# Kernel tuning notes

Measured on AMD Instinct MI355X. Metric: run time of the kernel, lower is better.

The kernel has to match this reference:

```python
import jax, jax.numpy as jnp
import numpy as np

B, N, D, H, F = 2, 2048, 1024, 16, 4096
E = D // H
EPS = 1e-5

def layer_norm(x, g, b):
    mu = jnp.mean(x, axis=-1, keepdims=True)
    var = jnp.var(x, axis=-1, keepdims=True)
    return (x - mu) * jax.lax.rsqrt(var + EPS) * g + b

def setup_inputs() -> dict:
    key = jax.random.key(0)
    ks = jax.random.split(key, 16)
    s = lambda k, sh, fan: jax.random.normal(k, sh, jnp.float32) * (1.0 / np.sqrt(fan))
    return {
        'x': jax.random.normal(ks[0], (B, N, D), jnp.float32),
        'wq': s(ks[1], (D, D), D), 'bq': jnp.zeros((D,), jnp.float32),
        'wk': s(ks[2], (D, D), D), 'bk': jnp.zeros((D,), jnp.float32),
        'wv': s(ks[3], (D, D), D), 'bv': jnp.zeros((D,), jnp.float32),
        'w1': s(ks[4], (F, D), D), 'b1': jnp.zeros((F,), jnp.float32),
        'ln_mlp_g': jnp.ones((F,), jnp.float32), 'ln_mlp_b': jnp.zeros((F,), jnp.float32),
        'w2': s(ks[5], (D, F), F), 'b2': jnp.zeros((D,), jnp.float32),
        'ln1_g': jnp.ones((D,), jnp.float32), 'ln1_b': jnp.zeros((D,), jnp.float32),
        'ln2_g': jnp.ones((D,), jnp.float32), 'ln2_b': jnp.zeros((D,), jnp.float32),
    }

def reference(x, wq, bq, wk, bk, wv, bv, w1, b1, ln_mlp_g, ln_mlp_b, w2, b2, ln1_g, ln1_b, ln2_g, ln2_b):
    h = layer_norm(x, ln1_g, ln1_b)                       # [B,N,D]
    q = (h @ wq.T + bq).reshape(B, N, H, E).transpose(0, 2, 1, 3)  # [B,H,N,E]
    k = (h @ wk.T + bk).reshape(B, N, H, E).transpose(0, 2, 1, 3)
    v = (h @ wv.T + bv).reshape(B, N, H, E).transpose(0, 2, 1, 3)
    # faithful to source: score = q@k^T / sqrt(1/emb_dim) == q@k^T * sqrt(emb_dim)
    score = jnp.einsum('bhne,bhme->bhnm', q, k) * np.sqrt(D).astype(np.float32)
    causal = jnp.tril(jnp.ones((N, N), bool))
    score = jnp.where(causal[None, None], score, -jnp.inf)
    weight = jax.nn.softmax(score, axis=-1)
    attn = jnp.einsum('bhnm,bhme->bhne', weight, v)       # [B,H,N,E]
    attn = attn.transpose(0, 2, 1, 3).reshape(B, N, D)
    x = x + attn
    h2 = layer_norm(x, ln2_g, ln2_b)
    m = h2 @ w1.T + b1                                    # [B,N,F]
    m = jax.nn.relu(layer_norm(m, ln_mlp_g, ln_mlp_b))
    # faithful: no second residual in the source forward
    return m @ w2.T + b2
```

## Files before the change

kernel.cpp:

```cpp
#include <hip/hip_runtime.h>
#include <cstdint>

typedef __bf16 bf16_t;
typedef bf16_t bf16x8 __attribute__((ext_vector_type(8)));
typedef bf16_t bf16x4 __attribute__((ext_vector_type(4)));
typedef float  floatx4 __attribute__((ext_vector_type(4)));

#define GLD_LDS(g, l) __builtin_amdgcn_global_load_lds( \
    (const __attribute__((address_space(1))) unsigned int*)(g), \
    (__attribute__((address_space(3))) unsigned int*)(l), 16, 0, 0)

#define MFMA_BF16_16x16x32 __builtin_amdgcn_mfma_f32_16x16x32_bf16

__global__ __launch_bounds__(256) void prep(
    const float* __restrict__ wq, const float* __restrict__ wk,
    const float* __restrict__ wv, const float* __restrict__ w1,
    const float* __restrict__ w2, const float* __restrict__ bq,
    const float* __restrict__ bk,
    bf16_t* __restrict__ wqk_hi, bf16_t* __restrict__ wqk_lo,
    bf16_t* __restrict__ wvb, bf16_t* __restrict__ w1b, bf16_t* __restrict__ w2b,
    float* __restrict__ bqk) {
  const int blk = blockIdx.x, tid = threadIdx.x;
  if (blk < 2048) {
    const int qk = blk >> 10;
    const int i  = (blk & 1023) * 256 + tid;
    const float* src = qk ? wk : wq;
    float4 v = ((const float4*)src)[i];
    float f[4] = {v.x, v.y, v.z, v.w};
    bf16x4 h, l;
    #pragma unroll
    for (int j = 0; j < 4; ++j) { h[j] = (bf16_t)f[j]; l[j] = (bf16_t)(f[j] - (float)h[j]); }
    ((bf16x4*)(wqk_hi + qk * 1024 * 1024))[i] = h;
    ((bf16x4*)(wqk_lo + qk * 1024 * 1024))[i] = l;
  } else if (blk < 3072) {
    const int i = (blk - 2048) * 256 + tid;
    float4 v = ((const float4*)wv)[i];
    bf16x4 o; o[0]=(bf16_t)v.x; o[1]=(bf16_t)v.y; o[2]=(bf16_t)v.z; o[3]=(bf16_t)v.w;
    ((bf16x4*)wvb)[i] = o;
  } else if (blk < 7168) {
    const int i = (blk - 3072) * 256 + tid;
    float4 v = ((const float4*)w1)[i];
    bf16x4 o; o[0]=(bf16_t)v.x; o[1]=(bf16_t)v.y; o[2]=(bf16_t)v.z; o[3]=(bf16_t)v.w;
    ((bf16x4*)w1b)[i] = o;
  } else if (blk < 11264) {
    const int i = (blk - 7168) * 256 + tid;
    float4 v = ((const float4*)w2)[i];
    bf16x4 o; o[0]=(bf16_t)v.x; o[1]=(bf16_t)v.y; o[2]=(bf16_t)v.z; o[3]=(bf16_t)v.w;
    ((bf16x4*)w2b)[i] = o;
  } else {
    const int i = (blk - 11264) * 256 + tid;
    if (i < 1024) { bqk[i] = bq[i]; bqk[1024 + i] = bk[i]; }
  }
}


__device__ __forceinline__ void block_sum2(float& s, float& ss, float* red) {
  #pragma unroll
  for (int off = 32; off > 0; off >>= 1) {
    s  += __shfl_down(s, off);
    ss += __shfl_down(ss, off);
  }
  const int wave = threadIdx.x >> 6;
  if ((threadIdx.x & 63) == 0) { red[wave * 2] = s; red[wave * 2 + 1] = ss; }
  __syncthreads();
  s  = red[0] + red[2] + red[4] + red[6];
  ss = red[1] + red[3] + red[5] + red[7];
}

__global__ __launch_bounds__(256) void ln_fwd_split(const float* __restrict__ x,
    const float* __restrict__ g, const float* __restrict__ b,
    bf16_t* __restrict__ out_hi, bf16_t* __restrict__ out_lo) {
  __shared__ float red[8];
  const size_t row = blockIdx.x;
  float4 v = ((const float4*)(x + row * 1024))[threadIdx.x];
  float s  = v.x + v.y + v.z + v.w;
  float ss = v.x*v.x + v.y*v.y + v.z*v.z + v.w*v.w;
  block_sum2(s, ss, red);
  const float mu  = s * (1.f / 1024.f);
  const float var = ss * (1.f / 1024.f) - mu * mu;
  const float rs  = rsqrtf(var + 1e-5f);
  float4 gg = ((const float4*)g)[threadIdx.x];
  float4 bb = ((const float4*)b)[threadIdx.x];
  float f[4];
  f[0] = (v.x - mu) * rs * gg.x + bb.x;
  f[1] = (v.y - mu) * rs * gg.y + bb.y;
  f[2] = (v.z - mu) * rs * gg.z + bb.z;
  f[3] = (v.w - mu) * rs * gg.w + bb.w;
  bf16x4 oh, ol;
  #pragma unroll
  for (int j = 0; j < 4; ++j) {
    oh[j] = (bf16_t)f[j];
    ol[j] = (bf16_t)(f[j] - (float)oh[j]);
  }
  ((bf16x4*)(out_hi + row * 1024))[threadIdx.x] = oh;
  ((bf16x4*)(out_lo + row * 1024))[threadIdx.x] = ol;
}

__global__ __launch_bounds__(256) void resid_ln_fwd(const float* __restrict__ x,
    const float* __restrict__ a, const float* __restrict__ g, const float* __restrict__ b,
    bf16_t* __restrict__ out) {
  __shared__ float red[8];
  const size_t row = blockIdx.x;
  float4 v = ((const float4*)(x + row * 1024))[threadIdx.x];
  float4 av = ((const float4*)(a + row * 1024))[threadIdx.x];
  v.x += av.x; v.y += av.y; v.z += av.z; v.w += av.w;
  float s  = v.x + v.y + v.z + v.w;
  float ss = v.x*v.x + v.y*v.y + v.z*v.z + v.w*v.w;
  block_sum2(s, ss, red);
  const float mu  = s * (1.f / 1024.f);
  const float var = ss * (1.f / 1024.f) - mu * mu;
  const float rs  = rsqrtf(var + 1e-5f);
  float4 gg = ((const float4*)g)[threadIdx.x];
  float4 bb = ((const float4*)b)[threadIdx.x];
  bf16x4 o;
  o[0] = (bf16_t)((v.x - mu) * rs * gg.x + bb.x);
  o[1] = (bf16_t)((v.y - mu) * rs * gg.y + bb.y);
  o[2] = (bf16_t)((v.z - mu) * rs * gg.z + bb.z);
  o[3] = (bf16_t)((v.w - mu) * rs * gg.w + bb.w);
  ((bf16x4*)(out + row * 1024))[threadIdx.x] = o;
}

__global__ __launch_bounds__(256) void ln_relu_inplace(bf16_t* __restrict__ m,
    const float* __restrict__ g, const float* __restrict__ b) {
  __shared__ float red[8];
  const size_t row = blockIdx.x;
  bf16_t* mr = m + row * 4096;
  const int base = threadIdx.x * 16;
  bf16x8 v0 = *(bf16x8*)(mr + base);
  bf16x8 v1 = *(bf16x8*)(mr + base + 8);
  float f[16];
  #pragma unroll
  for (int i = 0; i < 8; ++i) { f[i] = (float)v0[i]; f[8 + i] = (float)v1[i]; }
  float s = 0.f, ss = 0.f;
  #pragma unroll
  for (int i = 0; i < 16; ++i) { s += f[i]; ss += f[i] * f[i]; }
  block_sum2(s, ss, red);
  const float mu  = s * (1.f / 4096.f);
  const float var = ss * (1.f / 4096.f) - mu * mu;
  const float rs  = rsqrtf(var + 1e-5f);
  bf16x8 o0, o1;
  #pragma unroll
  for (int i = 0; i < 16; ++i) {
    float ov = (f[i] - mu) * rs * g[base + i] + b[base + i];
    ov = fmaxf(ov, 0.f);
    if (i < 8) o0[i] = (bf16_t)ov; else o1[i - 8] = (bf16_t)ov;
  }
  *(bf16x8*)(mr + base) = o0;
  *(bf16x8*)(mr + base + 8) = o1;
}

__device__ __forceinline__ void xcd_chunk2d(int& bx, int& by) {
  const int gx = gridDim.x;
  const int f  = (int)(blockIdx.y * gx + blockIdx.x);
  const int xcd = f & 7;
  const int i = f >> 3;
  const int bxPer = gx >> 3;
  by = i / bxPer;
  bx = xcd * bxPer + (i - by * bxPer);
}

template <int OUT_MODE, int BM, int SK>
__global__ __launch_bounds__(256) void gemm_bt(
    const bf16_t* __restrict__ A, const bf16_t* __restrict__ Bw,
    const float* __restrict__ bias, void* __restrict__ Cp,
    int M, int N, int K) {
  constexpr int MI = BM / 32;
  constexpr int ASZ = BM * 32;
  constexpr int BSZ = 128 * 32;
  __shared__ bf16_t As[2 * ASZ];
  __shared__ bf16_t Bs[2 * BSZ];
  const int tid  = threadIdx.x;
  const int wave = tid >> 6, lane = tid & 63;
  const int quad = lane >> 4, l15 = lane & 15;
  int bx = blockIdx.x, by = blockIdx.y;
  xcd_chunk2d(bx, by);
  const int m0 = bx * BM, n0 = by * 128;
  const int wm = (wave >> 1) * (BM / 2), wn = (wave & 1) * 64;
  const int srowA = wave * (BM / 4) + (lane >> 2);
  const int srowB = wave * 32 + (lane >> 2);
  const int scol = (lane & 3) * 8;
  const int ks = (SK > 1) ? (int)blockIdx.z : 0;
  const int kbeg = ks * (K / SK), kend = kbeg + K / SK;

  floatx4 acc[MI][4] = {};

  const bf16_t* Ag = A  + (size_t)(m0 + srowA) * K + scol;
  const bf16_t* Bg = Bw + (size_t)(n0 + srowB) * K + scol;

  auto stage = [&](int buf, int k0) {
    #pragma unroll
    for (int i = 0; i < BM / 64; ++i)
      GLD_LDS(Ag + (size_t)(i * 16) * K + k0,
              As + buf * ASZ + wave * (BM / 4) * 32 + i * 512);
    #pragma unroll
    for (int i = 0; i < 2; ++i)
      GLD_LDS(Bg + (size_t)(i * 16) * K + k0,
              Bs + buf * BSZ + wave * 1024 + i * 512);
  };

  stage(0, kbeg);
  __syncthreads();
  int cur = 0;
  for (int k0 = kbeg; k0 < kend; k0 += 32) {
    if (k0 + 32 < kend) stage(cur ^ 1, k0 + 32);
    bf16x8 af[MI], bfr[4];
    #pragma unroll
    for (int i = 0; i < MI; ++i)
      af[i] = *(const bf16x8*)(As + cur * ASZ + (wm + i * 16 + l15) * 32 + quad * 8);
    #pragma unroll
    for (int j = 0; j < 4; ++j)
      bfr[j] = *(const bf16x8*)(Bs + cur * BSZ + (wn + j * 16 + l15) * 32 + quad * 8);
    #pragma unroll
    for (int i = 0; i < MI; ++i)
      #pragma unroll
      for (int j = 0; j < 4; ++j)
        acc[i][j] = MFMA_BF16_16x16x32(af[i], bfr[j], acc[i][j], 0, 0, 0);
    __syncthreads();
    cur ^= 1;
  }
  if (OUT_MODE == 3) {
    #pragma unroll
    for (int j = 0; j < 4; ++j) {
      const int col = n0 + wn + j * 16 + l15;
      const float bv = bias[col];
      const int h = col >> 6, e = col & 63;
      #pragma unroll
      for (int i = 0; i < MI; ++i) {
        const int row0 = m0 + wm + i * 16 + quad * 4;
        const int b = row0 >> 11, n = row0 & 2047;
        bf16x4 o;
        #pragma unroll
        for (int r = 0; r < 4; ++r) o[r] = (bf16_t)(acc[i][j][r] + bv);
        *(bf16x4*)((bf16_t*)Cp + ((size_t)((b << 4) + h) * 64 + e) * 2048 + n) = o;
      }
    }
    return;
  }
  #pragma unroll
  for (int j = 0; j < 4; ++j) {
    const int col = n0 + wn + j * 16 + l15;
    const float bv = (SK == 1 || ks == 0) ? bias[col] : 0.f;
    #pragma unroll
    for (int i = 0; i < MI; ++i) {
      #pragma unroll
      for (int r = 0; r < 4; ++r) {
        const int row = m0 + wm + i * 16 + quad * 4 + r;
        const float v = acc[i][j][r] + bv;
        if (OUT_MODE == 0) {
          if (SK > 1) atomicAdd(&((float*)Cp)[(size_t)row * N + col], v);
          else        ((float*)Cp)[(size_t)row * N + col] = v;
        } else if (OUT_MODE == 1) {
          ((bf16_t*)Cp)[(size_t)row * N + col] = (bf16_t)v;
        }
      }
    }
  }
}

__global__ __launch_bounds__(256) void gemm_qk_split(
    const bf16_t* __restrict__ Ah, const bf16_t* __restrict__ Al,
    const bf16_t* __restrict__ Bh, const bf16_t* __restrict__ Bl,
    const float* __restrict__ bias,
    bf16_t* __restrict__ qhi, bf16_t* __restrict__ qlo,
    bf16_t* __restrict__ khi, bf16_t* __restrict__ klo,
    int M, int N, int K) {
  __shared__ bf16_t Ash[64 * 32];
  __shared__ bf16_t Asl[64 * 32];
  __shared__ bf16_t Bsh[128 * 32];
  __shared__ bf16_t Bsl[128 * 32];
  const int tid  = threadIdx.x;
  const int wave = tid >> 6, lane = tid & 63;
  const int quad = lane >> 4, l15 = lane & 15;
  int bx = blockIdx.x, by = blockIdx.y;
  xcd_chunk2d(bx, by);
  const int m0 = bx * 64, n0 = by * 128;
  const int wm = (wave >> 1) * 32, wn = (wave & 1) * 64;
  const int srowA = wave * 16 + (lane >> 2);
  const int srowB = wave * 32 + (lane >> 2);
  const int scol = (lane & 3) * 8;

  floatx4 acc[2][4] = {};

  const size_t aoff = (size_t)(m0 + srowA) * K + scol;
  const size_t boff = (size_t)(n0 + srowB) * K + scol;

  for (int k0 = 0; k0 < K; k0 += 32) {
    __syncthreads();
    GLD_LDS(Ah + aoff + k0, Ash + wave * 512);
    GLD_LDS(Al + aoff + k0, Asl + wave * 512);
    #pragma unroll
    for (int i = 0; i < 2; ++i) {
      const size_t gb = boff + (size_t)(i * 16) * K + k0;
      GLD_LDS(Bh + gb, Bsh + wave * 1024 + i * 512);
      GLD_LDS(Bl + gb, Bsl + wave * 1024 + i * 512);
    }
    __syncthreads();
    bf16x8 ah[2], al[2], bh[4], bl[4];
    #pragma unroll
    for (int i = 0; i < 2; ++i) {
      const int ro = (wm + i * 16 + l15) * 32 + quad * 8;
      ah[i] = *(const bf16x8*)(Ash + ro);
      al[i] = *(const bf16x8*)(Asl + ro);
    }
    #pragma unroll
    for (int j = 0; j < 4; ++j) {
      const int ro = (wn + j * 16 + l15) * 32 + quad * 8;
      bh[j] = *(const bf16x8*)(Bsh + ro);
      bl[j] = *(const bf16x8*)(Bsl + ro);
    }
    #pragma unroll
    for (int i = 0; i < 2; ++i)
      #pragma unroll
      for (int j = 0; j < 4; ++j) {
        acc[i][j] = MFMA_BF16_16x16x32(ah[i], bh[j], acc[i][j], 0, 0, 0);
        acc[i][j] = MFMA_BF16_16x16x32(ah[i], bl[j], acc[i][j], 0, 0, 0);
        acc[i][j] = MFMA_BF16_16x16x32(al[i], bh[j], acc[i][j], 0, 0, 0);
      }
  }
  #pragma unroll
  for (int j = 0; j < 4; ++j) {
    const int col = n0 + wn + j * 16 + l15;
    const float bv = bias[col];
    const bool isq = col < 1024;
    bf16_t* hib = isq ? qhi : khi;
    bf16_t* lob = isq ? qlo : klo;
    const float scale = isq ? 32.0f : 1.0f;
    const int h = (col >> 6) & 15, e = col & 63;
    #pragma unroll
    for (int i = 0; i < 2; ++i) {
      #pragma unroll
      for (int r = 0; r < 4; ++r) {
        const int row = m0 + wm + i * 16 + quad * 4 + r;
        const int b = row >> 11, n = row & 2047;
        const float c = (acc[i][j][r] + bv) * scale;
        const bf16_t chi = (bf16_t)c;
        const bf16_t clo = (bf16_t)(c - (float)chi);
        const size_t dst = (((size_t)((b << 4) + h) * 2048 + n) << 6) + e;
        hib[dst] = chi;
        lob[dst] = clo;
      }
    }
  }
}

#define SWZ(row, chunk) (((row) << 6) + ((((chunk) ^ ((row) & 7))) << 3))
__global__ __launch_bounds__(256, 4) void attn_causal(
    const bf16_t* __restrict__ qhi, const bf16_t* __restrict__ qlo,
    const bf16_t* __restrict__ khi, const bf16_t* __restrict__ klo,
    const bf16_t* __restrict__ vT, float* __restrict__ o) {
  __shared__ bf16_t KsH[64 * 64];
  __shared__ bf16_t KsL[64 * 64];
  __shared__ bf16_t Vt[64 * 64];
  __shared__ bf16_t Ps[4][16 * 64];

  const int tid  = threadIdx.x;
  const int wave = tid >> 6, lane = tid & 63;
  const int quad = lane >> 4, l15 = lane & 15;
  const int bh = blockIdx.x;
  const int q0 = (31 - (int)blockIdx.y) * 64;
  const size_t hb = (size_t)bh * 2048;

  const int wmin = q0 + wave * 16;
  const int qrow = wmin + l15;
  bf16x8 qh[2], ql[2];
  {
    const bf16_t* qbh = qhi + ((hb + wmin + l15) << 6) + quad * 8;
    const bf16_t* qbl = qlo + ((hb + wmin + l15) << 6) + quad * 8;
    qh[0] = *(const bf16x8*)qbh;
    qh[1] = *(const bf16x8*)(qbh + 32);
    ql[0] = *(const bf16x8*)qbl;
    ql[1] = *(const bf16x8*)(qbl + 32);
  }

  floatx4 accO[4] = {};
  float m_row = -1e30f;
  float l_row = 0.f;

  const int kr = wave * 16 + (lane >> 3);
  const int kc7 = lane & 7;
  const bf16_t* kgh = khi + ((hb + kr) << 6) + kc7 * 8;
  const bf16_t* kgl = klo + ((hb + kr) << 6) + kc7 * 8;
  const bf16_t* vg  = vT + ((size_t)(bh * 64 + kr)) * 2048 + kc7 * 8;

  bf16x8 pkh0 = *(const bf16x8*)(kgh);
  bf16x8 pkh1 = *(const bf16x8*)(kgh + (8 << 6));
  bf16x8 pkl0 = *(const bf16x8*)(kgl);
  bf16x8 pkl1 = *(const bf16x8*)(kgl + (8 << 6));
  bf16x8 pv0  = *(const bf16x8*)(vg);
  bf16x8 pv1  = *(const bf16x8*)(vg + 8 * 2048);

  const int ntiles = (q0 >> 6) + 1;
  for (int t = 0; t < ntiles; ++t) {
    const int k0 = t * 64;
    __syncthreads();
    *(bf16x8*)(KsH + SWZ(kr, kc7))     = pkh0;
    *(bf16x8*)(KsH + SWZ(kr + 8, kc7)) = pkh1;
    *(bf16x8*)(KsL + SWZ(kr, kc7))     = pkl0;
    *(bf16x8*)(KsL + SWZ(kr + 8, kc7)) = pkl1;
    *(bf16x8*)(Vt  + SWZ(kr, kc7))     = pv0;
    *(bf16x8*)(Vt  + SWZ(kr + 8, kc7)) = pv1;
    if (t + 1 < ntiles) {
      const int koff = (t + 1) << 12;
      pkh0 = *(const bf16x8*)(kgh + koff);
      pkh1 = *(const bf16x8*)(kgh + koff + (8 << 6));
      pkl0 = *(const bf16x8*)(kgl + koff);
      pkl1 = *(const bf16x8*)(kgl + koff + (8 << 6));
      pv0  = *(const bf16x8*)(vg + (t + 1) * 64);
      pv1  = *(const bf16x8*)(vg + (t + 1) * 64 + 8 * 2048);
    }
    __syncthreads();

    const bool needmask = (k0 + 63 > wmin);

    floatx4 sv[4];
    __builtin_amdgcn_s_setprio(1);
    #pragma unroll
    for (int j = 0; j < 4; ++j) {
      const int rK = j * 16 + l15;
      const bf16x8 kh0 = *(const bf16x8*)(KsH + SWZ(rK, quad));
      const bf16x8 kh1 = *(const bf16x8*)(KsH + SWZ(rK, quad + 4));
      const bf16x8 kl0 = *(const bf16x8*)(KsL + SWZ(rK, quad));
      const bf16x8 kl1 = *(const bf16x8*)(KsL + SWZ(rK, quad + 4));
      floatx4 acc = {};
      acc = MFMA_BF16_16x16x32(kh0, qh[0], acc, 0, 0, 0);
      acc = MFMA_BF16_16x16x32(kh1, qh[1], acc, 0, 0, 0);
      acc = MFMA_BF16_16x16x32(kl0, qh[0], acc, 0, 0, 0);
      acc = MFMA_BF16_16x16x32(kl1, qh[1], acc, 0, 0, 0);
      acc = MFMA_BF16_16x16x32(kh0, ql[0], acc, 0, 0, 0);
      acc = MFMA_BF16_16x16x32(kh1, ql[1], acc, 0, 0, 0);
      sv[j] = acc;
    }
    __builtin_amdgcn_s_setprio(0);

    const int lim = qrow - k0 - quad * 4;
    float mr = -1e30f;
    #pragma unroll
    for (int j = 0; j < 4; ++j)
      #pragma unroll
      for (int r = 0; r < 4; ++r) {
        float x = sv[j][r];
        if (needmask && (j * 16 + r > lim)) x = -1e30f;
        sv[j][r] = x;
        mr = fmaxf(mr, x);
      }
    mr = fmaxf(mr, __shfl_xor(mr, 16));
    mr = fmaxf(mr, __shfl_xor(mr, 32));
    const float mold = m_row;
    const float mnew = fmaxf(mold, mr);
    m_row = mnew;
    float psum = 0.f;
    bf16x4 pb[4];
    #pragma unroll
    for (int j = 0; j < 4; ++j)
      #pragma unroll
      for (int r = 0; r < 4; ++r) {
        const float p = __expf(sv[j][r] - mnew);
        const bf16_t pv = (bf16_t)p;
        psum += (float)pv;
        pb[j][r] = pv;
      }
    {
      bf16_t* pw = &Ps[wave][0];
      #pragma unroll
      for (int j = 0; j < 4; ++j)
        *(bf16x4*)(pw + SWZ(l15, 2 * j + (quad >> 1)) + (quad & 1) * 4) = pb[j];
    }
    psum += __shfl_xor(psum, 16);
    psum += __shfl_xor(psum, 32);
    const float alpha = __expf(mold - mnew);
    l_row = l_row * alpha + psum;
    if (__any(mnew > mold)) {
      #pragma unroll
      for (int r = 0; r < 4; ++r) {
        const float ar = __shfl(alpha, quad * 4 + r);
        #pragma unroll
        for (int j = 0; j < 4; ++j) accO[j][r] *= ar;
      }
    }
    asm volatile("s_waitcnt lgkmcnt(0)" ::: "memory");
    __builtin_amdgcn_sched_barrier(0);

    bf16x8 pf[2];
    {
      const bf16_t* pw = &Ps[wave][0];
      pf[0] = *(const bf16x8*)(pw + SWZ(l15, quad));
      pf[1] = *(const bf16x8*)(pw + SWZ(l15, quad + 4));
    }
    __builtin_amdgcn_s_setprio(1);
    #pragma unroll
    for (int j = 0; j < 4; ++j) {
      const int rV = j * 16 + l15;
      const bf16x8 vf0 = *(const bf16x8*)(Vt + SWZ(rV, quad));
      const bf16x8 vf1 = *(const bf16x8*)(Vt + SWZ(rV, quad + 4));
      accO[j] = MFMA_BF16_16x16x32(pf[0], vf0, accO[j], 0, 0, 0);
      accO[j] = MFMA_BF16_16x16x32(pf[1], vf1, accO[j], 0, 0, 0);
    }
    __builtin_amdgcn_s_setprio(0);
  }

  const int b = bh >> 4, h = bh & 15;
  #pragma unroll
  for (int r = 0; r < 4; ++r) {
    const float lr = __shfl(l_row, quad * 4 + r);
    const float linv = 1.f / lr;
    const int qr = wmin + quad * 4 + r;
    float* orow = o + ((size_t)(b * 2048) + qr) * 1024 + h * 64;
    #pragma unroll
    for (int j = 0; j < 4; ++j)
      orow[j * 16 + l15] = accO[j][r] * linv;
  }
}


extern "C" void kernel_launch(void* const* d_in, const int* in_sizes, int n_in,
                              void* d_out, int out_size, void* d_ws, size_t ws_size,
                              hipStream_t stream) {
  const float* x        = (const float*)d_in[0];
  const float* wq       = (const float*)d_in[1];
  const float* bq       = (const float*)d_in[2];
  const float* wk       = (const float*)d_in[3];
  const float* bk       = (const float*)d_in[4];
  const float* wv       = (const float*)d_in[5];
  const float* bv       = (const float*)d_in[6];
  const float* w1       = (const float*)d_in[7];
  const float* b1       = (const float*)d_in[8];
  const float* ln_mlp_g = (const float*)d_in[9];
  const float* ln_mlp_b = (const float*)d_in[10];
  const float* w2       = (const float*)d_in[11];
  const float* b2       = (const float*)d_in[12];
  const float* ln1_g    = (const float*)d_in[13];
  const float* ln1_b    = (const float*)d_in[14];
  const float* ln2_g    = (const float*)d_in[15];
  const float* ln2_b    = (const float*)d_in[16];

  char* ws = (char*)d_ws;
  bf16_t* h_hi   = (bf16_t*)(ws);
  bf16_t* h_lo   = (bf16_t*)(ws + (8u  << 20));
  bf16_t* wqk_hi = (bf16_t*)(ws + (16u << 20));
  bf16_t* wqk_lo = (bf16_t*)(ws + (20u << 20));
  bf16_t* wvb    = (bf16_t*)(ws + (24u << 20));
  float*  bqk    = (float*) (ws + (26u << 20));
  bf16_t* w1b    = (bf16_t*)(ws + (28u << 20));
  bf16_t* w2b    = (bf16_t*)(ws + (36u << 20));
  bf16_t* qhi    = (bf16_t*)(ws + (44u << 20));
  bf16_t* qlo    = (bf16_t*)(ws + (52u << 20));
  bf16_t* khi    = (bf16_t*)(ws + (60u << 20));
  bf16_t* klo    = (bf16_t*)(ws + (68u << 20));
  bf16_t* mbuf   = (bf16_t*)(ws + (44u << 20));
  bf16_t* vTb    = (bf16_t*)(ws + (76u << 20));
  float*  attnb  = (float*) (ws + (84u << 20));
  bf16_t* h2     = (bf16_t*)(ws + (100u << 20));

  hipMemsetAsync(d_out, 0, (size_t)4096 * 1024 * sizeof(float), stream);

  prep<<<11268, 256, 0, stream>>>(wq, wk, wv, w1, w2, bq, bk,
                                  wqk_hi, wqk_lo, wvb, w1b, w2b, bqk);

  ln_fwd_split<<<4096, 256, 0, stream>>>(x, ln1_g, ln1_b, h_hi, h_lo);
  gemm_qk_split<<<dim3(64, 16), 256, 0, stream>>>(h_hi, h_lo, wqk_hi, wqk_lo, bqk,
                                                  qhi, qlo, khi, klo, 4096, 2048, 1024);
  gemm_bt<3, 64, 1><<<dim3(64, 8), 256, 0, stream>>>(h_hi, wvb, bv, vTb, 4096, 1024, 1024);
  attn_causal<<<dim3(32, 32), 256, 0, stream>>>(qhi, qlo, khi, klo, vTb, attnb);
  resid_ln_fwd<<<4096, 256, 0, stream>>>(x, attnb, ln2_g, ln2_b, h2);
  gemm_bt<1, 128, 1><<<dim3(32, 32), 256, 0, stream>>>(h2, w1b, b1, mbuf, 4096, 4096, 1024);
  ln_relu_inplace<<<4096, 256, 0, stream>>>(mbuf, ln_mlp_g, ln_mlp_b);
  gemm_bt<0, 64, 2><<<dim3(64, 8, 2), 256, 0, stream>>>(mbuf, w2b, b2, d_out, 4096, 1024, 4096);

  (void)in_sizes; (void)n_in; (void)out_size; (void)ws_size;
}
```

Baseline: 431.3 us.

## Add single-buffered BK=64 GEMM path with XOR-swizzled LDS layout

Adds a BK=64 variant of gemm_bt that stages 64-wide K tiles into single-buffered shared memory using an XOR-swizzled chunk layout, then runs two MFMA sub-steps per tile. The V projection and the split-K down projection now use this path, while the up projection keeps the double-buffered BK=32 loop. The aim is to halve the number of K iterations and barriers and to cut LDS bank conflicts. In exchange the new path gives up load/compute overlap, since it syncs before and after every tile.

```diff
diff --git a/kernel.cpp b/kernel.cpp
--- a/kernel.cpp
+++ b/kernel.cpp
@@ -159,16 +159,17 @@
   bx = xcd * bxPer + (i - by * bxPer);
 }
 
-template <int OUT_MODE, int BM, int SK>
+template <int OUT_MODE, int BM, int SK, int BK>
 __global__ __launch_bounds__(256) void gemm_bt(
     const bf16_t* __restrict__ A, const bf16_t* __restrict__ Bw,
     const float* __restrict__ bias, void* __restrict__ Cp,
     int M, int N, int K) {
   constexpr int MI = BM / 32;
-  constexpr int ASZ = BM * 32;
-  constexpr int BSZ = 128 * 32;
-  __shared__ bf16_t As[2 * ASZ];
-  __shared__ bf16_t Bs[2 * BSZ];
+  constexpr bool DB = (BK == 32);
+  constexpr int ASZ = BM * BK;
+  constexpr int BSZ = 128 * BK;
+  __shared__ bf16_t As[(DB ? 2 : 1) * ASZ];
+  __shared__ bf16_t Bs[(DB ? 2 : 1) * BSZ];
   const int tid  = threadIdx.x;
   const int wave = tid >> 6, lane = tid & 63;
   const int quad = lane >> 4, l15 = lane & 15;
@@ -176,48 +177,84 @@
   xcd_chunk2d(bx, by);
   const int m0 = bx * BM, n0 = by * 128;
   const int wm = (wave >> 1) * (BM / 2), wn = (wave & 1) * 64;
-  const int srowA = wave * (BM / 4) + (lane >> 2);
-  const int srowB = wave * 32 + (lane >> 2);
-  const int scol = (lane & 3) * 8;
   const int ks = (SK > 1) ? (int)blockIdx.z : 0;
   const int kbeg = ks * (K / SK), kend = kbeg + K / SK;
 
   floatx4 acc[MI][4] = {};
 
-  const bf16_t* Ag = A  + (size_t)(m0 + srowA) * K + scol;
-  const bf16_t* Bg = Bw + (size_t)(n0 + srowB) * K + scol;
-
-  auto stage = [&](int buf, int k0) {
-    #pragma unroll
-    for (int i = 0; i < BM / 64; ++i)
-      GLD_LDS(Ag + (size_t)(i * 16) * K + k0,
-              As + buf * ASZ + wave * (BM / 4) * 32 + i * 512);
-    #pragma unroll
-    for (int i = 0; i < 2; ++i)
-      GLD_LDS(Bg + (size_t)(i * 16) * K + k0,
-              Bs + buf * BSZ + wave * 1024 + i * 512);
-  };
-
-  stage(0, kbeg);
-  __syncthreads();
-  int cur = 0;
-  for (int k0 = kbeg; k0 < kend; k0 += 32) {
-    if (k0 + 32 < kend) stage(cur ^ 1, k0 + 32);
-    bf16x8 af[MI], bfr[4];
-    #pragma unroll
-    for (int i = 0; i < MI; ++i)
-      af[i] = *(const bf16x8*)(As + cur * ASZ + (wm + i * 16 + l15) * 32 + quad * 8);
-    #pragma unroll
-    for (int j = 0; j < 4; ++j)
-      bfr[j] = *(const bf16x8*)(Bs + cur * BSZ + (wn + j * 16 + l15) * 32 + quad * 8);
-    #pragma unroll
-    for (int i = 0; i < MI; ++i)
+  if constexpr (BK == 32) {
+    const int srowA = wave * (BM / 4) + (lane >> 2);
+    const int srowB = wave * 32 + (lane >> 2);
+    const int scol = (lane & 3) * 8;
+    const bf16_t* Ag = A  + (size_t)(m0 + srowA) * K + scol;
+    const bf16_t* Bg = Bw + (size_t)(n0 + srowB) * K + scol;
+    auto stage = [&](int buf, int k0) {
+      #pragma unroll
+      for (int i = 0; i < BM / 64; ++i)
+        GLD_LDS(Ag + (size_t)(i * 16) * K + k0,
+                As + buf * ASZ + wave * (BM / 4) * 32 + i * 512);
+      #pragma unroll
+      for (int i = 0; i < 2; ++i)
+        GLD_LDS(Bg + (size_t)(i * 16) * K + k0,
+                Bs + buf * BSZ + wave * 1024 + i * 512);
+    };
+    stage(0, kbeg);
+    __syncthreads();
+    int cur = 0;
+    for (int k0 = kbeg; k0 < kend; k0 += 32) {
+      if (k0 + 32 < kend) stage(cur ^ 1, k0 + 32);
+      bf16x8 af[MI], bfr[4];
+      #pragma unroll
+      for (int i = 0; i < MI; ++i)
+        af[i] = *(const bf16x8*)(As + cur * ASZ + (wm + i * 16 + l15) * 32 + quad * 8);
       #pragma unroll
       for (int j = 0; j < 4; ++j)
-        acc[i][j] = MFMA_BF16_16x16x32(af[i], bfr[j], acc[i][j], 0, 0, 0);
-    __syncthreads();
-    cur ^= 1;
-  }
+        bfr[j] = *(const bf16x8*)(Bs + cur * BSZ + (wn + j * 16 + l15) * 32 + quad * 8);
+      #pragma unroll
+      for (int i = 0; i < MI; ++i)
+        #pragma unroll
+        for (int j = 0; j < 4; ++j)
+          acc[i][j] = MFMA_BF16_16x16x32(af[i], bfr[j], acc[i][j], 0, 0, 0);
+      __syncthreads();
+      cur ^= 1;
+    }
+  } else {
+    for (int k0 = kbeg; k0 < kend; k0 += 64) {
+      __syncthreads();
+      #pragma unroll
+      for (int i = 0; i < BM / 32; ++i) {
+        const int flat = i * 64 + lane;
+        const int rl = flat >> 3, ch = flat & 7;
+        GLD_LDS(A + (size_t)(m0 + wave * (BM / 4) + rl) * K + k0 + ((ch ^ (rl & 7)) * 8),
+                As + wave * (BM / 4) * 64 + i * 512);
+      }
+      #pragma unroll
+      for (int i = 0; i < 4; ++i) {
+        const int flat = i * 64 + lane;
+        const int rl = flat >> 3, ch = flat & 7;
+        GLD_LDS(Bw + (size_t)(n0 + wave * 32 + rl) * K + k0 + ((ch ^ (rl & 7)) * 8),
+                Bs + wave * 32 * 64 + i * 512);
+      }
+      __syncthreads();
+      #pragma unroll
+      for (int kk = 0; kk < 2; ++kk) {
+        const int co = ((quad + 4 * kk) ^ (l15 & 7)) * 8;
+        bf16x8 af[MI], bfr[4];
+        #pragma unroll
+        for (int i = 0; i < MI; ++i)
+          af[i] = *(const bf16x8*)(As + (wm + i * 16 + l15) * 64 + co);
+        #pragma unroll
+        for (int j = 0; j < 4; ++j)
+          bfr[j] = *(const bf16x8*)(Bs + (wn + j * 16 + l15) * 64 + co);
+        #pragma unroll
+        for (int i = 0; i < MI; ++i)
+          #pragma unroll
+          for (int j = 0; j < 4; ++j)
+            acc[i][j] = MFMA_BF16_16x16x32(af[i], bfr[j], acc[i][j], 0, 0, 0);
+      }
+    }
+  }
+
   if (OUT_MODE == 3) {
     #pragma unroll
     for (int j = 0; j < 4; ++j) {
@@ -559,12 +596,12 @@
   ln_fwd_split<<<4096, 256, 0, stream>>>(x, ln1_g, ln1_b, h_hi, h_lo);
   gemm_qk_split<<<dim3(64, 16), 256, 0, stream>>>(h_hi, h_lo, wqk_hi, wqk_lo, bqk,
                                                   qhi, qlo, khi, klo, 4096, 2048, 1024);
-  gemm_bt<3, 64, 1><<<dim3(64, 8), 256, 0, stream>>>(h_hi, wvb, bv, vTb, 4096, 1024, 1024);
+  gemm_bt<3, 64, 1, 64><<<dim3(64, 8), 256, 0, stream>>>(h_hi, wvb, bv, vTb, 4096, 1024, 1024);
   attn_causal<<<dim3(32, 32), 256, 0, stream>>>(qhi, qlo, khi, klo, vTb, attnb);
   resid_ln_fwd<<<4096, 256, 0, stream>>>(x, attnb, ln2_g, ln2_b, h2);
-  gemm_bt<1, 128, 1><<<dim3(32, 32), 256, 0, stream>>>(h2, w1b, b1, mbuf, 4096, 4096, 1024);
+  gemm_bt<1, 128, 1, 32><<<dim3(32, 32), 256, 0, stream>>>(h2, w1b, b1, mbuf, 4096, 4096, 1024);
   ln_relu_inplace<<<4096, 256, 0, stream>>>(mbuf, ln_mlp_g, ln_mlp_b);
-  gemm_bt<0, 64, 2><<<dim3(64, 8, 2), 256, 0, stream>>>(mbuf, w2b, b2, d_out, 4096, 1024, 4096);
+  gemm_bt<0, 64, 2, 64><<<dim3(64, 8, 2), 256, 0, stream>>>(mbuf, w2b, b2, d_out, 4096, 1024, 4096);
 
   (void)in_sizes; (void)n_in; (void)out_size; (void)ws_size;
 }
```

Measured after the change: 405.3 us. 6.0% less time.
